# Performance work log

Hardware: AMD Instinct MI355X
Metric: run time of the kernel (lower is better)

## Reference

```python
import jax, jax.numpy as jnp
import numpy as np

N, D, C = 16384, 64, 128
MARGIN = 1.0
EPS_NORM = 1e-6   # F.normalize eps
EPS_PD = 1e-6     # F.pairwise_distance eps (added to the difference elementwise)


def setup_inputs() -> dict:
    key = jax.random.key(0)
    embeddings = jax.random.normal(key, (N, D), dtype=jnp.float32)
    labels = (jnp.arange(N) % C).astype(jnp.int32).reshape(N, 1)
    # deterministic valid positive: same label (i % C), different index
    pos_idx = ((jnp.arange(N) + C) % N).astype(jnp.int32)
    return {"embeddings": embeddings, "labels": labels, "pos_idx": pos_idx}


def reference(embeddings, labels, pos_idx):
    # L2-normalize rows (torch F.normalize: x / max(||x||, eps))
    nrm = jnp.linalg.norm(embeddings, axis=1, keepdims=True)
    e = embeddings / jnp.maximum(nrm, EPS_NORM)

    lab = labels[:, 0]
    # torch pairwise_distance computes ||x1 - x2 + eps||_2, eps added per element:
    # ||xi - xj + eps||^2 = ||xi||^2 + ||xj||^2 - 2 xi.xj + 2*eps*(sum(xi)-sum(xj)) + D*eps^2
    sq = jnp.sum(e * e, axis=1)          # [N]
    s = jnp.sum(e, axis=1)               # [N]
    gram = e @ e.T                        # [N, N]
    d2 = (sq[:, None] + sq[None, :] - 2.0 * gram
          + 2.0 * EPS_PD * (s[:, None] - s[None, :]) + D * EPS_PD * EPS_PD)
    d2 = jnp.maximum(d2, 0.0)
    dist = jnp.sqrt(jnp.maximum(d2, 1e-12))  # guard sqrt grad at 0

    # one positive per anchor: squared distance
    pos_loss = jnp.sum(d2[jnp.arange(N), pos_idx])

    # all negatives per anchor: hinge^2 on (margin - dist)
    neg_mask = lab[:, None] != lab[None, :]
    hinge = jnp.maximum(MARGIN - dist, 0.0)
    neg_loss = jnp.sum(jnp.where(neg_mask, hinge * hinge, 0.0))

    n_comparisons = N + jnp.sum(neg_mask)
    return (pos_loss + neg_loss) / n_comparisons.astype(jnp.float32)
```

## Files before the change

kernel.cpp:

```cpp
#include <hip/hip_runtime.h>
#include <hip/hip_bf16.h>

#define NN 16384
#define DD 64
#define NBI 32
#define NUNITS 2112
#define NBLK 768
#define NPOSB (NN/4)
#define RING 3
#define SCREEN_T 0.49f

constexpr float F_EPS_PD   = 1e-6f;
constexpr float F_EPS_NORM = 1e-6f;

using bf16x8 = __attribute__((ext_vector_type(8))) short;
using f32x4  = __attribute__((ext_vector_type(4))) float;
typedef __attribute__((address_space(1))) const unsigned int gu32_t;
typedef __attribute__((address_space(3))) unsigned int       lu32_t;

__device__ __forceinline__ float wave_sum_f(float v) {
    #pragma unroll
    for (int o = 32; o >= 1; o >>= 1) v += __shfl_xor(v, o);
    return v;
}

__device__ __forceinline__ int band_off(int I) { return 2 * I * (65 - I); }

__global__ __launch_bounds__(256) void norm_kernel(
    const float* __restrict__ emb, const int* __restrict__ pidx,
    const int* __restrict__ lab, float* __restrict__ u,
    float2* __restrict__ vcp, __hip_bfloat16* __restrict__ ebf,
    float* __restrict__ posP) {
    int w    = threadIdx.x >> 6;
    int row  = blockIdx.x * 4 + w;
    int lane = threadIdx.x & 63;
    int j    = pidx[row];
    float x  = emb[(size_t)row * DD + lane];
    float xj = emb[(size_t)j   * DD + lane];

    float n2  = wave_sum_f(x * x);
    float sx  = wave_sum_f(x);
    float n2j = wave_sum_f(xj * xj);
    float sxj = wave_sum_f(xj);
    float dot = wave_sum_f(x * xj);

    float m  = fmaxf(sqrtf(n2),  F_EPS_NORM);
    float mj = fmaxf(sqrtf(n2j), F_EPS_NORM);
    ebf[(size_t)row * DD + lane] = __float2bfloat16(x / m);

    __shared__ float spos[4];
    if (lane == 0) {
        float sq  = n2 / (m * m);
        float sqj = n2j / (mj * mj);
        float s   = sx / m;
        float sj  = sxj / mj;
        float g   = dot / (m * mj);
        u[row] = sq + 2.0f * F_EPS_PD * s;
        vcp[row] = make_float2(
            sq - 2.0f * F_EPS_PD * s + (float)DD * F_EPS_PD * F_EPS_PD,
            (float)lab[row]);
        float d2p = sq + sqj - 2.0f * g + 2.0f * F_EPS_PD * (s - sj)
                  + (float)DD * F_EPS_PD * F_EPS_PD;
        spos[w] = fmaxf(d2p, 0.0f);
    }
    __syncthreads();
    if (threadIdx.x == 0)
        posP[blockIdx.x] = spos[0] + spos[1] + spos[2] + spos[3];
}

__device__ __forceinline__ void stage_tile(const short* tbase, short* slot,
                                           int w, int lane) {
    int rlo = lane >> 3;
    int g   = (lane & 7) ^ rlo;
    #pragma unroll
    for (int q = 0; q < 2; ++q) {
        int m = w * 2 + q;
        __builtin_amdgcn_global_load_lds(
            (gu32_t*)(const void*)(tbase + (size_t)(8 * m + rlo) * DD + g * 8),
            (lu32_t*)(void*)(slot + m * 512), 16, 0, 0);
    }
}

__global__ __launch_bounds__(512, 4) void pair_kernel(
    const short* __restrict__ ebf, const float* __restrict__ u,
    const float2* __restrict__ vcp, float* __restrict__ negP) {
    __shared__ short ring[RING][8192];
    __shared__ float sred[8];
    int tid  = threadIdx.x;
    int w    = tid >> 6;
    int lane = tid & 63;
    int lrow = lane & 15, lkh = lane >> 4;
    int c0s  = ((lkh)     ^ (lrow & 7)) * 8;
    int c1s  = ((lkh + 4) ^ (lrow & 7)) * 8;

    int ks = (int)(((long long)blockIdx.x * NUNITS) / NBLK);
    int ke = (int)(((long long)(blockIdx.x + 1) * NUNITS) / NBLK);

    int I = (int)((65.0f - sqrtf(4225.0f - 2.0f * (float)ks)) * 0.5f);
    I = I < 0 ? 0 : (I > NBI - 1 ? NBI - 1 : I);
    while (band_off(I) > ks) --I;
    while (I < NBI - 1 && band_off(I + 1) <= ks) ++I;

    float hacc = 0.0f;
    int k0 = ks;
    while (k0 < ke) {
        int bend = band_off(I + 1);
        int n    = (ke < bend ? ke : bend) - k0;
        int tj0  = 4 * I + (k0 - band_off(I));
        int rowbase = I * 512 + w * 64;
        int rt      = 4 * I + (w >> 1);

        bf16x8 a[4][2];
        float uo[4][4], lo[4][4];
        #pragma unroll
        for (int s = 0; s < 4; ++s) {
            const short* ab = ebf + (size_t)(rowbase + 16 * s + lrow) * DD + lkh * 8;
            a[s][0] = *(const bf16x8*)(ab);
            a[s][1] = *(const bf16x8*)(ab + 32);
            #pragma unroll
            for (int r = 0; r < 4; ++r) {
                int i0 = rowbase + 16 * s + lkh * 4 + r;
                uo[s][r] = u[i0];
                lo[s][r] = vcp[i0].y;
            }
        }
        int np = n < 2 ? n : 2;
        for (int p = 0; p < np; ++p)
            stage_tile(ebf + (size_t)(tj0 + p) * (128 * DD), &ring[p][0], w, lane);

        for (int k = 0; k < n; ++k) {
            if (k + 1 < n) asm volatile("s_waitcnt vmcnt(2)" ::: "memory");
            else           asm volatile("s_waitcnt vmcnt(0)" ::: "memory");
            __builtin_amdgcn_s_barrier();
            __builtin_amdgcn_sched_barrier(0);
            if (k + 2 < n)
                stage_tile(ebf + (size_t)(tj0 + k + 2) * (128 * DD),
                           &ring[(k + 2) % RING][0], w, lane);

            int tj = tj0 + k;
            float wgt = (tj == rt) ? 1.0f : ((tj > rt) ? 2.0f : 0.0f);
            if (wgt != 0.0f) {
                const short* sl = &ring[k % RING][0];
                int bj = tj * 128;
                float hp = 0.0f;
                #pragma unroll
                for (int t = 0; t < 8; ++t) {
                    const short* rowp = sl + (t * 16 + lrow) * 64;
                    bf16x8 b0 = *(const bf16x8*)(rowp + c0s);
                    bf16x8 b1 = *(const bf16x8*)(rowp + c1s);
                    f32x4 c[4];
                    #pragma unroll
                    for (int s = 0; s < 4; ++s) {
                        f32x4 z = {0.f, 0.f, 0.f, 0.f};
                        z = __builtin_amdgcn_mfma_f32_16x16x32_bf16(a[s][0], b0, z, 0, 0, 0);
                        z = __builtin_amdgcn_mfma_f32_16x16x32_bf16(a[s][1], b1, z, 0, 0, 0);
                        c[s] = z;
                    }
                    float mx = fmaxf(fmaxf(c[0][0], c[0][1]), fmaxf(c[0][2], c[0][3]));
                    mx = fmaxf(mx, fmaxf(fmaxf(c[1][0], c[1][1]), fmaxf(c[1][2], c[1][3])));
                    mx = fmaxf(mx, fmaxf(fmaxf(c[2][0], c[2][1]), fmaxf(c[2][2], c[2][3])));
                    mx = fmaxf(mx, fmaxf(fmaxf(c[3][0], c[3][1]), fmaxf(c[3][2], c[3][3])));
                    if (__any(mx > SCREEN_T)) {
                        float2 vl = vcp[bj + t * 16 + lrow];
                        #pragma unroll
                        for (int s = 0; s < 4; ++s) {
                            #pragma unroll
                            for (int r = 0; r < 4; ++r) {
                                float d2 = fmaf(-2.0f, c[s][r], uo[s][r] + vl.x);
                                float d  = sqrtf(fmaxf(d2, 1e-12f));
                                float h  = fmaxf(1.0f - d, 0.0f);
                                if (lo[s][r] != vl.y) hp = fmaf(h, h, hp);
                            }
                        }
                    }
                }
                hacc = fmaf(wgt, hp, hacc);
            }
        }
        __builtin_amdgcn_s_barrier();
        k0 += n;
        ++I;
    }

    hacc = wave_sum_f(hacc);
    if (lane == 0) sred[w] = hacc;
    __syncthreads();
    if (tid == 0) {
        float tn = 0.f;
        #pragma unroll
        for (int i = 0; i < 8; ++i) tn += sred[i];
        negP[blockIdx.x] = tn;
    }
}

__global__ __launch_bounds__(256) void reduce_kernel(
    const float* __restrict__ posP, const float* __restrict__ negP,
    const int* __restrict__ lab, float* __restrict__ out) {
    __shared__ unsigned int hist[1024];
    int t = threadIdx.x;
    for (int i = t; i < 1024; i += 256) hist[i] = 0u;
    __syncthreads();
    const int4* lab4 = (const int4*)lab;
    for (int i = t; i < NN / 4; i += 256) {
        int4 v = lab4[i];
        atomicAdd(&hist[v.x & 1023], 1u);
        atomicAdd(&hist[v.y & 1023], 1u);
        atomicAdd(&hist[v.z & 1023], 1u);
        atomicAdd(&hist[v.w & 1023], 1u);
    }
    __syncthreads();

    float ps = 0.f, ns = 0.f;
    unsigned int sqc = 0u;
    const float4* posP4 = (const float4*)posP;
    for (int i = t; i < NPOSB / 4; i += 256) {
        float4 v = posP4[i];
        ps += (v.x + v.y) + (v.z + v.w);
    }
    for (int i = t; i < NBLK; i += 256) ns += negP[i];
    for (int i = t; i < 1024; i += 256) { unsigned int h = hist[i]; sqc += h * h; }

    ps = wave_sum_f(ps);
    ns = wave_sum_f(ns);
    #pragma unroll
    for (int o = 32; o >= 1; o >>= 1) sqc += __shfl_xor(sqc, o);

    __shared__ float sp[4], sn[4];
    __shared__ unsigned int sc[4];
    int w = t >> 6, lane = t & 63;
    if (lane == 0) { sp[w] = ps; sn[w] = ns; sc[w] = sqc; }
    __syncthreads();
    if (t == 0) {
        float pos = sp[0] + sp[1] + sp[2] + sp[3];
        float neg = sn[0] + sn[1] + sn[2] + sn[3];
        unsigned long long s2 = (unsigned long long)sc[0] + sc[1] + sc[2] + sc[3];
        unsigned long long nneg = (unsigned long long)NN * NN - s2;
        float ncomp = (float)((unsigned long long)NN + nneg);
        out[0] = (pos + neg) / ncomp;
    }
}

extern "C" void kernel_launch(void* const* d_in, const int* in_sizes, int n_in,
                              void* d_out, int out_size, void* d_ws, size_t ws_size,
                              hipStream_t stream) {
    const float* emb = (const float*)d_in[0];
    const int* lab   = (const int*)d_in[1];
    const int* pidx  = (const int*)d_in[2];
    float* out = (float*)d_out;
    char* ws = (char*)d_ws;
    float*          u    = (float*)(ws);
    float2*         vcp  = (float2*)(ws + 65536);
    __hip_bfloat16* ebf  = (__hip_bfloat16*)(ws + 196608);
    float*          posP = (float*)(ws + 2293760);
    float*          negP = (float*)(ws + 2310144);

    norm_kernel<<<NPOSB, 256, 0, stream>>>(emb, pidx, lab, u, vcp, ebf, posP);
    pair_kernel<<<NBLK, 512, 0, stream>>>((const short*)ebf, u, vcp, negP);
    reduce_kernel<<<1, 256, 0, stream>>>(posP, negP, lab, out);
}
```

Measured before the change: 57.96 us.

## Stage column norms/labels into LDS, pack row data, cut block count to 512

The pair kernel now stages each column tile's norm/label pairs into LDS alongside the bf16 tile through the async global-to-LDS path. It also loads the band's row norms and labels into a shared buffer instead of holding 32 of them in registers. The grid shrinks from 768 to 512 blocks, and the reduction kernel widens to 1024 threads with per-wave private histograms. The aim is to remove scattered global loads in the screened epilogue and lower register pressure. In exchange, LDS use per block grows, the epilogue gains extra LDS reads, and fewer blocks may leave load imbalance.

New measurement: 53.85 us. 7.1% less time.

```diff
diff --git a/kernel.cpp b/kernel.cpp
--- a/kernel.cpp
+++ b/kernel.cpp
@@ -5,9 +5,8 @@
 #define DD 64
 #define NBI 32
 #define NUNITS 2112
-#define NBLK 768
+#define NBLK 512
 #define NPOSB (NN/4)
-#define RING 3
 #define SCREEN_T 0.49f
 
 constexpr float F_EPS_PD   = 1e-6f;
@@ -28,7 +27,7 @@
 
 __global__ __launch_bounds__(256) void norm_kernel(
     const float* __restrict__ emb, const int* __restrict__ pidx,
-    const int* __restrict__ lab, float* __restrict__ u,
+    const int* __restrict__ lab, float2* __restrict__ up,
     float2* __restrict__ vcp, __hip_bfloat16* __restrict__ ebf,
     float* __restrict__ posP) {
     int w    = threadIdx.x >> 6;
@@ -55,10 +54,10 @@
         float s   = sx / m;
         float sj  = sxj / mj;
         float g   = dot / (m * mj);
-        u[row] = sq + 2.0f * F_EPS_PD * s;
+        float lf  = (float)lab[row];
+        up[row]  = make_float2(sq + 2.0f * F_EPS_PD * s, lf);
         vcp[row] = make_float2(
-            sq - 2.0f * F_EPS_PD * s + (float)DD * F_EPS_PD * F_EPS_PD,
-            (float)lab[row]);
+            sq - 2.0f * F_EPS_PD * s + (float)DD * F_EPS_PD * F_EPS_PD, lf);
         float d2p = sq + sqj - 2.0f * g + 2.0f * F_EPS_PD * (s - sj)
                   + (float)DD * F_EPS_PD * F_EPS_PD;
         spos[w] = fmaxf(d2p, 0.0f);
@@ -68,8 +67,10 @@
         posP[blockIdx.x] = spos[0] + spos[1] + spos[2] + spos[3];
 }
 
-__device__ __forceinline__ void stage_tile(const short* tbase, short* slot,
+__device__ __forceinline__ void stage_tile(const short* ebf, const float2* vcp,
+                                           int tile, short* slotB, float2* slotV,
                                            int w, int lane) {
+    const short* tbase = ebf + (size_t)tile * (128 * DD);
     int rlo = lane >> 3;
     int g   = (lane & 7) ^ rlo;
     #pragma unroll
@@ -77,15 +78,20 @@
         int m = w * 2 + q;
         __builtin_amdgcn_global_load_lds(
             (gu32_t*)(const void*)(tbase + (size_t)(8 * m + rlo) * DD + g * 8),
-            (lu32_t*)(void*)(slot + m * 512), 16, 0, 0);
-    }
+            (lu32_t*)(void*)(slotB + m * 512), 16, 0, 0);
+    }
+    __builtin_amdgcn_global_load_lds(
+        (gu32_t*)(const void*)(vcp + (size_t)tile * 128 + lane * 2),
+        (lu32_t*)(void*)slotV, 16, 0, 0);
 }
 
 __global__ __launch_bounds__(512, 4) void pair_kernel(
-    const short* __restrict__ ebf, const float* __restrict__ u,
+    const short* __restrict__ ebf, const float2* __restrict__ up,
     const float2* __restrict__ vcp, float* __restrict__ negP) {
-    __shared__ short ring[RING][8192];
-    __shared__ float sred[8];
+    __shared__ short  ringB[3][8192];
+    __shared__ float2 ringV[3][128];
+    __shared__ float2 uband[512];
+    __shared__ float  sred[8];
     int tid  = threadIdx.x;
     int w    = tid >> 6;
     int lane = tid & 63;
@@ -102,83 +108,85 @@
     while (I < NBI - 1 && band_off(I + 1) <= ks) ++I;
 
     float hacc = 0.0f;
-    int k0 = ks;
-    while (k0 < ke) {
+    int u0 = ks;
+    while (u0 < ke) {
         int bend = band_off(I + 1);
-        int n    = (ke < bend ? ke : bend) - k0;
-        int tj0  = 4 * I + (k0 - band_off(I));
+        int n    = (ke < bend ? ke : bend) - u0;
+        int tj0  = 4 * I + (u0 - band_off(I));
         int rowbase = I * 512 + w * 64;
         int rt      = 4 * I + (w >> 1);
 
         bf16x8 a[4][2];
-        float uo[4][4], lo[4][4];
         #pragma unroll
         for (int s = 0; s < 4; ++s) {
             const short* ab = ebf + (size_t)(rowbase + 16 * s + lrow) * DD + lkh * 8;
             a[s][0] = *(const bf16x8*)(ab);
             a[s][1] = *(const bf16x8*)(ab + 32);
-            #pragma unroll
-            for (int r = 0; r < 4; ++r) {
-                int i0 = rowbase + 16 * s + lkh * 4 + r;
-                uo[s][r] = u[i0];
-                lo[s][r] = vcp[i0].y;
-            }
         }
-        int np = n < 2 ? n : 2;
-        for (int p = 0; p < np; ++p)
-            stage_tile(ebf + (size_t)(tj0 + p) * (128 * DD), &ring[p][0], w, lane);
-
+        if (w < 4)
+            __builtin_amdgcn_global_load_lds(
+                (gu32_t*)(const void*)(up + (size_t)I * 512 + w * 128 + lane * 2),
+                (lu32_t*)(void*)(uband + w * 128), 16, 0, 0);
+        stage_tile(ebf, vcp, tj0, &ringB[0][0], &ringV[0][0], w, lane);
+        if (n > 1)
+            stage_tile(ebf, vcp, tj0 + 1, &ringB[1][0], &ringV[1][0], w, lane);
+
+        int sl = 0;
         for (int k = 0; k < n; ++k) {
-            if (k + 1 < n) asm volatile("s_waitcnt vmcnt(2)" ::: "memory");
+            if (k + 1 < n) asm volatile("s_waitcnt vmcnt(3)" ::: "memory");
             else           asm volatile("s_waitcnt vmcnt(0)" ::: "memory");
             __builtin_amdgcn_s_barrier();
             __builtin_amdgcn_sched_barrier(0);
+            int sl2 = (sl >= 1) ? sl - 1 : 2;
             if (k + 2 < n)
-                stage_tile(ebf + (size_t)(tj0 + k + 2) * (128 * DD),
-                           &ring[(k + 2) % RING][0], w, lane);
+                stage_tile(ebf, vcp, tj0 + k + 2, &ringB[sl2][0], &ringV[sl2][0],
+                           w, lane);
 
             int tj = tj0 + k;
             float wgt = (tj == rt) ? 1.0f : ((tj > rt) ? 2.0f : 0.0f);
             if (wgt != 0.0f) {
-                const short* sl = &ring[k % RING][0];
-                int bj = tj * 128;
+                const short*  lb = &ringB[sl][0];
+                const float2* lv = &ringV[sl][0];
                 float hp = 0.0f;
                 #pragma unroll
                 for (int t = 0; t < 8; ++t) {
-                    const short* rowp = sl + (t * 16 + lrow) * 64;
+                    const short* rowp = lb + (t * 16 + lrow) * 64;
                     bf16x8 b0 = *(const bf16x8*)(rowp + c0s);
                     bf16x8 b1 = *(const bf16x8*)(rowp + c1s);
-                    f32x4 c[4];
+                    f32x4 c4[4];
                     #pragma unroll
                     for (int s = 0; s < 4; ++s) {
                         f32x4 z = {0.f, 0.f, 0.f, 0.f};
                         z = __builtin_amdgcn_mfma_f32_16x16x32_bf16(a[s][0], b0, z, 0, 0, 0);
                         z = __builtin_amdgcn_mfma_f32_16x16x32_bf16(a[s][1], b1, z, 0, 0, 0);
-                        c[s] = z;
+                        c4[s] = z;
                     }
-                    float mx = fmaxf(fmaxf(c[0][0], c[0][1]), fmaxf(c[0][2], c[0][3]));
-                    mx = fmaxf(mx, fmaxf(fmaxf(c[1][0], c[1][1]), fmaxf(c[1][2], c[1][3])));
-                    mx = fmaxf(mx, fmaxf(fmaxf(c[2][0], c[2][1]), fmaxf(c[2][2], c[2][3])));
-                    mx = fmaxf(mx, fmaxf(fmaxf(c[3][0], c[3][1]), fmaxf(c[3][2], c[3][3])));
+                    float mx = fmaxf(fmaxf(c4[0][0], c4[0][1]), fmaxf(c4[0][2], c4[0][3]));
+                    mx = fmaxf(mx, fmaxf(fmaxf(c4[1][0], c4[1][1]), fmaxf(c4[1][2], c4[1][3])));
+                    mx = fmaxf(mx, fmaxf(fmaxf(c4[2][0], c4[2][1]), fmaxf(c4[2][2], c4[2][3])));
+                    mx = fmaxf(mx, fmaxf(fmaxf(c4[3][0], c4[3][1]), fmaxf(c4[3][2], c4[3][3])));
                     if (__any(mx > SCREEN_T)) {
-                        float2 vl = vcp[bj + t * 16 + lrow];
+                        float2 vl = lv[t * 16 + lrow];
                         #pragma unroll
                         for (int s = 0; s < 4; ++s) {
                             #pragma unroll
                             for (int r = 0; r < 4; ++r) {
-                                float d2 = fmaf(-2.0f, c[s][r], uo[s][r] + vl.x);
+                                float2 ul = uband[w * 64 + 16 * s + lkh * 4 + r];
+                                float d2 = fmaf(-2.0f, c4[s][r], ul.x + vl.x);
                                 float d  = sqrtf(fmaxf(d2, 1e-12f));
                                 float h  = fmaxf(1.0f - d, 0.0f);
-                                if (lo[s][r] != vl.y) hp = fmaf(h, h, hp);
+                                if (ul.y != vl.y) hp = fmaf(h, h, hp);
                             }
                         }
                     }
                 }
                 hacc = fmaf(wgt, hp, hacc);
             }
+            sl = (sl + 1 == 3) ? 0 : sl + 1;
         }
         __builtin_amdgcn_s_barrier();
-        k0 += n;
+        __builtin_amdgcn_sched_barrier(0);
+        u0 += n;
         ++I;
     }
 
@@ -193,47 +201,52 @@
     }
 }
 
-__global__ __launch_bounds__(256) void reduce_kernel(
+__global__ __launch_bounds__(1024) void reduce_kernel(
     const float* __restrict__ posP, const float* __restrict__ negP,
     const int* __restrict__ lab, float* __restrict__ out) {
-    __shared__ unsigned int hist[1024];
+    __shared__ unsigned int hist[4][1024];
     int t = threadIdx.x;
-    for (int i = t; i < 1024; i += 256) hist[i] = 0u;
+    int w = t >> 6, lane = t & 63;
+    for (int i = t; i < 4096; i += 1024) hist[i >> 10][i & 1023] = 0u;
     __syncthreads();
     const int4* lab4 = (const int4*)lab;
-    for (int i = t; i < NN / 4; i += 256) {
+    for (int i = t; i < NN / 4; i += 1024) {
         int4 v = lab4[i];
-        atomicAdd(&hist[v.x & 1023], 1u);
-        atomicAdd(&hist[v.y & 1023], 1u);
-        atomicAdd(&hist[v.z & 1023], 1u);
-        atomicAdd(&hist[v.w & 1023], 1u);
+        atomicAdd(&hist[w & 3][v.x & 1023], 1u);
+        atomicAdd(&hist[w & 3][v.y & 1023], 1u);
+        atomicAdd(&hist[w & 3][v.z & 1023], 1u);
+        atomicAdd(&hist[w & 3][v.w & 1023], 1u);
     }
     __syncthreads();
 
     float ps = 0.f, ns = 0.f;
-    unsigned int sqc = 0u;
+    unsigned long long sqc = 0u;
     const float4* posP4 = (const float4*)posP;
-    for (int i = t; i < NPOSB / 4; i += 256) {
+    for (int i = t; i < NPOSB / 4; i += 1024) {
         float4 v = posP4[i];
         ps += (v.x + v.y) + (v.z + v.w);
     }
-    for (int i = t; i < NBLK; i += 256) ns += negP[i];
-    for (int i = t; i < 1024; i += 256) { unsigned int h = hist[i]; sqc += h * h; }
+    if (t < NBLK) ns = negP[t];
+    for (int i = t; i < 1024; i += 1024) {
+        unsigned long long h = (unsigned long long)hist[0][i] + hist[1][i]
+                             + hist[2][i] + hist[3][i];
+        sqc += h * h;
+    }
 
     ps = wave_sum_f(ps);
     ns = wave_sum_f(ns);
     #pragma unroll
     for (int o = 32; o >= 1; o >>= 1) sqc += __shfl_xor(sqc, o);
 
-    __shared__ float sp[4], sn[4];
-    __shared__ unsigned int sc[4];
-    int w = t >> 6, lane = t & 63;
+    __shared__ float sp[16], sn[16];
+    __shared__ unsigned long long sc[16];
     if (lane == 0) { sp[w] = ps; sn[w] = ns; sc[w] = sqc; }
     __syncthreads();
     if (t == 0) {
-        float pos = sp[0] + sp[1] + sp[2] + sp[3];
-        float neg = sn[0] + sn[1] + sn[2] + sn[3];
-        unsigned long long s2 = (unsigned long long)sc[0] + sc[1] + sc[2] + sc[3];
+        float pos = 0.f, neg = 0.f;
+        unsigned long long s2 = 0;
+        #pragma unroll
+        for (int i = 0; i < 16; ++i) { pos += sp[i]; neg += sn[i]; s2 += sc[i]; }
         unsigned long long nneg = (unsigned long long)NN * NN - s2;
         float ncomp = (float)((unsigned long long)NN + nneg);
         out[0] = (pos + neg) / ncomp;
@@ -248,13 +261,13 @@
     const int* pidx  = (const int*)d_in[2];
     float* out = (float*)d_out;
     char* ws = (char*)d_ws;
-    float*          u    = (float*)(ws);
-    float2*         vcp  = (float2*)(ws + 65536);
-    __hip_bfloat16* ebf  = (__hip_bfloat16*)(ws + 196608);
-    float*          posP = (float*)(ws + 2293760);
-    float*          negP = (float*)(ws + 2310144);
-
-    norm_kernel<<<NPOSB, 256, 0, stream>>>(emb, pidx, lab, u, vcp, ebf, posP);
-    pair_kernel<<<NBLK, 512, 0, stream>>>((const short*)ebf, u, vcp, negP);
-    reduce_kernel<<<1, 256, 0, stream>>>(posP, negP, lab, out);
-}
+    float2*         up   = (float2*)(ws);
+    float2*         vcp  = (float2*)(ws + 131072);
+    __hip_bfloat16* ebf  = (__hip_bfloat16*)(ws + 262144);
+    float*          posP = (float*)(ws + 2359296);
+    float*          negP = (float*)(ws + 2375680);
+
+    norm_kernel<<<NPOSB, 256, 0, stream>>>(emb, pidx, lab, up, vcp, ebf, posP);
+    pair_kernel<<<NBLK, 512, 0, stream>>>((const short*)ebf, up, vcp, negP);
+    reduce_kernel<<<1, 1024, 0, stream>>>(posP, negP, lab, out);
+}
```
